# Performance work log

Hardware: AMD Instinct MI355X
Metric: run time of the kernel (lower is better)

Reference implementation:

```python
import jax, jax.numpy as jnp
import numpy as np

N_ACTIVE = 200000
GRID = 96
C_IN = 128
C_OUT = 128
K = 27  # 3x3x3 kernel offsets
BN_EPS = 1e-4  # scn.BatchNormalization default eps


def _build_rulebook(rng):
    """Sample N_ACTIVE unique voxels in a GRID^3 volume and build the
    submanifold-conv neighbor table: nbr_idx[k, i] = index of the active
    voxel at offset k from voxel i, or -1 if that site is inactive."""
    total = GRID ** 3
    flat = rng.choice(total, size=N_ACTIVE, replace=False).astype(np.int64)
    # flat -> dense lookup of active index
    lut = np.full(total, -1, dtype=np.int32)
    lut[flat] = np.arange(N_ACTIVE, dtype=np.int32)
    z = flat % GRID
    y = (flat // GRID) % GRID
    x = flat // (GRID * GRID)
    offs = np.array([(dx, dy, dz) for dx in (-1, 0, 1)
                     for dy in (-1, 0, 1) for dz in (-1, 0, 1)], dtype=np.int64)
    nbr = np.full((K, N_ACTIVE), -1, dtype=np.int32)
    for k, (dx, dy, dz) in enumerate(offs):
        nx, ny, nz = x + dx, y + dy, z + dz
        ok = ((nx >= 0) & (nx < GRID) & (ny >= 0) & (ny < GRID)
              & (nz >= 0) & (nz < GRID))
        nflat = np.where(ok, nx * GRID * GRID + ny * GRID + nz, 0)
        hit = np.where(ok, lut[nflat], -1)
        nbr[k] = hit
    return nbr


def setup_inputs() -> dict:
    key = jax.random.key(0)
    k1, k2 = jax.random.split(key)
    rng = np.random.default_rng(0)
    nbr_idx = jnp.asarray(_build_rulebook(rng))  # [27, N] int32
    features = jax.random.normal(k1, (N_ACTIVE, C_IN), dtype=jnp.float32)
    # Kaiming-ish scaled conv weights, one [Cin, Cout] matrix per offset
    W = jax.random.normal(k2, (K, C_IN, C_OUT), dtype=jnp.float32) * (
        1.0 / np.sqrt(K * C_IN))
    gamma = jnp.ones((C_OUT,), dtype=jnp.float32)
    beta = jnp.zeros((C_OUT,), dtype=jnp.float32)
    return {"features": features, "nbr_idx": nbr_idx, "W": W,
            "gamma": gamma, "beta": beta}


def reference(features, nbr_idx, W, gamma, beta):
    # --- Submanifold 3x3x3 convolution (gather -> GEMM -> accumulate) ---
    # Output sites == input sites; for each kernel offset k, gather the
    # neighbor's feature row (zero if inactive) and accumulate g @ W[k].
    out = jnp.zeros((features.shape[0], W.shape[-1]), dtype=features.dtype)
    for k in range(K):  # fixed small loop over 27 kernel offsets
        idx = nbr_idx[k]                         # [N]
        valid = (idx >= 0)
        g = features[jnp.maximum(idx, 0)]        # [N, Cin] irregular gather
        g = jnp.where(valid[:, None], g, 0.0)
        out = out + g @ W[k]                     # [N, Cout]
    # --- BatchNormalization over active sites (training batch stats) ---
    mean = jnp.mean(out, axis=0)
    var = jnp.mean(jnp.square(out - mean), axis=0)
    out = (out - mean) * (gamma * jax.lax.rsqrt(var + BN_EPS)) + beta
    # --- ReLU ---
    return jnp.maximum(out, 0.0)
```

## Files before the change

### kernel.cpp

```cpp
#include <hip/hip_runtime.h>
#include <hip/hip_bf16.h>
#include <cstdint>
#include <cstddef>

#define N_ACT 200000
#define CH 128
#define NOFF 27
#define TM 128

typedef __bf16 v8bf __attribute__((ext_vector_type(8)));
typedef float v4f __attribute__((ext_vector_type(4)));

__device__ __forceinline__ unsigned short f2bf(float f) {
    union { float f; unsigned int u; } x; x.f = f;
    unsigned int lsb = (x.u >> 16) & 1u;
    x.u += 0x7fffu + lsb;
    return (unsigned short)(x.u >> 16);
}

__global__ void cast_feat(const float* __restrict__ in,
                          unsigned short* __restrict__ out) {
    long long i = (long long)blockIdx.x * blockDim.x + threadIdx.x;
    long long base = i * 8;
    if (base >= (long long)N_ACT * CH) return;
    const float4* p = (const float4*)(in + base);
    float4 a = p[0], b = p[1];
    unsigned int w0 = (unsigned)f2bf(a.x) | ((unsigned)f2bf(a.y) << 16);
    unsigned int w1 = (unsigned)f2bf(a.z) | ((unsigned)f2bf(a.w) << 16);
    unsigned int w2 = (unsigned)f2bf(b.x) | ((unsigned)f2bf(b.y) << 16);
    unsigned int w3 = (unsigned)f2bf(b.z) | ((unsigned)f2bf(b.w) << 16);
    *(uint4*)(out + base) = make_uint4(w0, w1, w2, w3);
}

__global__ void prep_w(const float* __restrict__ W,
                       unsigned short* __restrict__ Wtp,
                       float* __restrict__ stats,
                       float* __restrict__ zpage) {
    int k = blockIdx.x;
    int t = threadIdx.x;
    if (k == 0 && t < 2 * CH) stats[t] = 0.0f;
    if (k == 0 && t < 64) zpage[t] = 0.0f;
    const float* wk = W + (size_t)k * CH * CH;
    for (int g = t; g < 2048; g += 256) {
        int q = g >> 9, r = g & 511;
        int jkk = r >> 6, lane = r & 63;
        int j = jkk >> 2, kk = jkk & 3;
        int lr = lane & 15, quad = lane >> 4;
        int cout = q * 32 + j * 16 + lr;
        int cin0 = kk * 32 + quad * 8;
        unsigned int wbuf[4];
        #pragma unroll
        for (int h = 0; h < 4; ++h) {
            unsigned short lo = f2bf(wk[(size_t)(cin0 + 2*h)     * CH + cout]);
            unsigned short hi = f2bf(wk[(size_t)(cin0 + 2*h + 1) * CH + cout]);
            wbuf[h] = (unsigned)lo | ((unsigned)hi << 16);
        }
        *(uint4*)(Wtp + ((size_t)(k * 4 + q) << 12) + (size_t)(jkk * 64 + lane) * 8)
            = make_uint4(wbuf[0], wbuf[1], wbuf[2], wbuf[3]);
    }
}

__global__ __launch_bounds__(256, 2) void conv_mfma(
        const unsigned short* __restrict__ feat,
        const int* __restrict__ nbr,
        const unsigned short* __restrict__ Wtp,
        const unsigned short* __restrict__ zpage,
        float* __restrict__ out,
        float* __restrict__ stats) {
    __shared__ __bf16 As[TM * CH];
    __shared__ int idxL[NOFF * TM];
    __shared__ float sred[256];

    const int t    = threadIdx.x;
    const int row0 = blockIdx.x * TM;
    const int wid  = t >> 6;
    const int lane = t & 63;
    const int lr   = lane & 15;
    const int quad = lane >> 4;

    for (int e = t; e < NOFF * TM; e += 256) {
        int k = e >> 7, r = e & 127;
        int gr = row0 + r;
        idxL[e] = (gr < N_ACT) ? nbr[(size_t)k * N_ACT + gr] : -1;
    }
    __syncthreads();

    v4f acc[8][2];
    #pragma unroll
    for (int i = 0; i < 8; ++i) {
        acc[i][0] = (v4f){0.f, 0.f, 0.f, 0.f};
        acc[i][1] = (v4f){0.f, 0.f, 0.f, 0.f};
    }

    const int sc  = t & 15;
    const int sr0 = t >> 4;
    const unsigned short* zsrc = zpage + sc * 8;

    v8bf B[8];

    auto stageA = [&](int k) {
        uint4 G[8];
        #pragma unroll
        for (int p = 0; p < 8; ++p) {
            int row = p * 16 + sr0;
            int idx = idxL[k * TM + row];
            const unsigned short* src =
                (idx >= 0) ? feat + ((size_t)idx << 7) + sc * 8 : zsrc;
            G[p] = *(const uint4*)src;
        }
        #pragma unroll
        for (int p = 0; p < 8; ++p) {
            int row = p * 16 + sr0;
            *(uint4*)(As + row * CH + (((sc + row) & 15) << 3)) = G[p];
        }
    };
    auto loadB = [&](int k) {
        const unsigned short* base =
            Wtp + ((size_t)(k * 4 + wid) << 12) + (size_t)lane * 8;
        #pragma unroll
        for (int jkk = 0; jkk < 8; ++jkk)
            B[jkk] = *(const v8bf*)(base + jkk * 512);
    };
    auto mfmaPhase = [&]() {
        #pragma unroll
        for (int i = 0; i < 8; ++i) {
            const __bf16* rowp = As + (i * 16 + lr) * CH;
            v8bf a[4];
            #pragma unroll
            for (int kk = 0; kk < 4; ++kk)
                a[kk] = *(const v8bf*)(rowp + (((kk * 4 + quad + lr) & 15) << 3));
            #pragma unroll
            for (int kk = 0; kk < 4; ++kk) {
                acc[i][0] = __builtin_amdgcn_mfma_f32_16x16x32_bf16(
                    a[kk], B[kk], acc[i][0], 0, 0, 0);
                acc[i][1] = __builtin_amdgcn_mfma_f32_16x16x32_bf16(
                    a[kk], B[4 + kk], acc[i][1], 0, 0, 0);
            }
        }
    };

    stageA(0);
    loadB(0);
    __syncthreads();

    #pragma unroll 1
    for (int k = 0; k < NOFF; ++k) {
        mfmaPhase();
        if (k + 1 < NOFF) {
            __syncthreads();
            stageA(k + 1);
            loadB(k + 1);
            __syncthreads();
        }
    }

    float psum[2] = {0.f, 0.f};
    float psq[2]  = {0.f, 0.f};
    #pragma unroll
    for (int i = 0; i < 8; ++i) {
        #pragma unroll
        for (int r = 0; r < 4; ++r) {
            int grow = row0 + i * 16 + quad * 4 + r;
            if (grow < N_ACT) {
                #pragma unroll
                for (int j = 0; j < 2; ++j) {
                    float v = acc[i][j][r];
                    out[(size_t)grow * CH + wid * 32 + j * 16 + lr] = v;
                    psum[j] += v;
                    psq[j]  += v * v;
                }
            }
        }
    }
    #pragma unroll
    for (int j = 0; j < 2; ++j) {
        psum[j] += __shfl_xor(psum[j], 16, 64);
        psq[j]  += __shfl_xor(psq[j], 16, 64);
        psum[j] += __shfl_xor(psum[j], 32, 64);
        psq[j]  += __shfl_xor(psq[j], 32, 64);
    }
    if (quad == 0) {
        #pragma unroll
        for (int j = 0; j < 2; ++j) {
            int c = wid * 32 + j * 16 + lr;
            sred[c]       = psum[j];
            sred[128 + c] = psq[j];
        }
    }
    __syncthreads();
    if (t < CH) {
        atomicAdd(&stats[t],      sred[t]);
        atomicAdd(&stats[CH + t], sred[128 + t]);
    }
}

__global__ void finalize_stats(const float* __restrict__ gamma,
                               const float* __restrict__ beta,
                               float* __restrict__ stats) {
    int c = threadIdx.x;
    if (c < CH) {
        float inv_n = 1.0f / (float)N_ACT;
        float mean  = stats[c] * inv_n;
        float var   = stats[CH + c] * inv_n - mean * mean;
        float sc    = gamma[c] * rsqrtf(var + 1e-4f);
        stats[2 * CH + c] = sc;
        stats[3 * CH + c] = beta[c] - mean * sc;
    }
}

__global__ void bn_relu(const float* __restrict__ conv,
                        const float* __restrict__ stats,
                        float* __restrict__ out) {
    long long i = (long long)blockIdx.x * blockDim.x + threadIdx.x;
    if (i >= (long long)N_ACT * CH / 4) return;
    int c4 = (int)(i & 31) * 4;
    float4 v  = ((const float4*)conv)[i];
    float4 sc = *(const float4*)(stats + 2 * CH + c4);
    float4 sh = *(const float4*)(stats + 3 * CH + c4);
    float4 o;
    o.x = fmaxf(v.x * sc.x + sh.x, 0.f);
    o.y = fmaxf(v.y * sc.y + sh.y, 0.f);
    o.z = fmaxf(v.z * sc.z + sh.z, 0.f);
    o.w = fmaxf(v.w * sc.w + sh.w, 0.f);
    ((float4*)out)[i] = o;
}

extern "C" void kernel_launch(void* const* d_in, const int* in_sizes, int n_in,
                              void* d_out, int out_size, void* d_ws, size_t ws_size,
                              hipStream_t stream) {
    const float* features = (const float*)d_in[0];
    const int*   nbr      = (const int*)d_in[1];
    const float* W        = (const float*)d_in[2];
    const float* gamma    = (const float*)d_in[3];
    const float* beta     = (const float*)d_in[4];
    float* outp = (float*)d_out;

    char* ws = (char*)d_ws;
    unsigned short* feat_bf = (unsigned short*)ws;
    unsigned short* Wtp     = (unsigned short*)(ws + 51200000);
    float* conv             = (float*)(ws + 51200000 + 884736);
    float* stats            = (float*)(ws + 51200000 + 884736 + 102400000);
    float* zpage            = stats + 4 * CH;

    cast_feat<<<12500, 256, 0, stream>>>(features, feat_bf);
    prep_w<<<NOFF, 256, 0, stream>>>(W, Wtp, stats, zpage);
    conv_mfma<<<(N_ACT + TM - 1) / TM, 256, 0, stream>>>(
        feat_bf, nbr, Wtp, (const unsigned short*)zpage, conv, stats);
    finalize_stats<<<1, CH, 0, stream>>>(gamma, beta, stats);
    bn_relu<<<25000, 256, 0, stream>>>(conv, stats, outp);
}
```

Baseline: 407.1 us.

## Retile conv MFMA warps to a 2x2 grid and use nontemporal output stores

Each of the four waves now computes a 64-row by 64-column tile instead of all 128 rows by 32 columns. That halves the per-wave LDS A-fragment reads while doubling the B fragments held in registers, and the per-block BN stat reduction is adjusted to sum over the two row halves. Separately, the conv output stores and the bn_relu load and store become nontemporal to reduce cache pollution on streaming data. The larger B register array (16 v8bf) plus 16 accumulators raises register pressure, which may threaten the 2-blocks-per-CU launch bound.

```diff
diff --git a/kernel.cpp b/kernel.cpp
--- a/kernel.cpp
+++ b/kernel.cpp
@@ -69,7 +69,7 @@
         float* __restrict__ stats) {
     __shared__ __bf16 As[TM * CH];
     __shared__ int idxL[NOFF * TM];
-    __shared__ float sred[256];
+    __shared__ float sred[512];
 
     const int t    = threadIdx.x;
     const int row0 = blockIdx.x * TM;
@@ -77,6 +77,8 @@
     const int lane = t & 63;
     const int lr   = lane & 15;
     const int quad = lane >> 4;
+    const int wr   = wid >> 1;
+    const int wc   = wid & 1;
 
     for (int e = t; e < NOFF * TM; e += 256) {
         int k = e >> 7, r = e & 127;
@@ -85,18 +87,18 @@
     }
     __syncthreads();
 
-    v4f acc[8][2];
+    v4f acc[4][4];
     #pragma unroll
-    for (int i = 0; i < 8; ++i) {
-        acc[i][0] = (v4f){0.f, 0.f, 0.f, 0.f};
-        acc[i][1] = (v4f){0.f, 0.f, 0.f, 0.f};
-    }
+    for (int i = 0; i < 4; ++i)
+        #pragma unroll
+        for (int j = 0; j < 4; ++j)
+            acc[i][j] = (v4f){0.f, 0.f, 0.f, 0.f};
 
     const int sc  = t & 15;
     const int sr0 = t >> 4;
     const unsigned short* zsrc = zpage + sc * 8;
 
-    v8bf B[8];
+    v8bf B[16];
 
     auto stageA = [&](int k) {
         uint4 G[8];
@@ -115,26 +117,30 @@
         }
     };
     auto loadB = [&](int k) {
-        const unsigned short* base =
-            Wtp + ((size_t)(k * 4 + wid) << 12) + (size_t)lane * 8;
-        #pragma unroll
-        for (int jkk = 0; jkk < 8; ++jkk)
-            B[jkk] = *(const v8bf*)(base + jkk * 512);
+        #pragma unroll
+        for (int j = 0; j < 4; ++j) {
+            const unsigned short* base = Wtp
+                + ((size_t)(k * 4 + 2 * wc + (j >> 1)) << 12)
+                + (size_t)(((j & 1) * 4) * 64 + lane) * 8;
+            #pragma unroll
+            for (int kk = 0; kk < 4; ++kk)
+                B[j * 4 + kk] = *(const v8bf*)(base + kk * 512);
+        }
     };
     auto mfmaPhase = [&]() {
         #pragma unroll
-        for (int i = 0; i < 8; ++i) {
-            const __bf16* rowp = As + (i * 16 + lr) * CH;
+        for (int i = 0; i < 4; ++i) {
+            const __bf16* rowp = As + (wr * 64 + i * 16 + lr) * CH;
             v8bf a[4];
             #pragma unroll
             for (int kk = 0; kk < 4; ++kk)
                 a[kk] = *(const v8bf*)(rowp + (((kk * 4 + quad + lr) & 15) << 3));
             #pragma unroll
             for (int kk = 0; kk < 4; ++kk) {
-                acc[i][0] = __builtin_amdgcn_mfma_f32_16x16x32_bf16(
-                    a[kk], B[kk], acc[i][0], 0, 0, 0);
-                acc[i][1] = __builtin_amdgcn_mfma_f32_16x16x32_bf16(
-                    a[kk], B[4 + kk], acc[i][1], 0, 0, 0);
+                #pragma unroll
+                for (int j = 0; j < 4; ++j)
+                    acc[i][j] = __builtin_amdgcn_mfma_f32_16x16x32_bf16(
+                        a[kk], B[j * 4 + kk], acc[i][j], 0, 0, 0);
             }
         }
     };
@@ -154,18 +160,19 @@
         }
     }
 
-    float psum[2] = {0.f, 0.f};
-    float psq[2]  = {0.f, 0.f};
+    float psum[4] = {0.f, 0.f, 0.f, 0.f};
+    float psq[4]  = {0.f, 0.f, 0.f, 0.f};
     #pragma unroll
-    for (int i = 0; i < 8; ++i) {
+    for (int i = 0; i < 4; ++i) {
         #pragma unroll
         for (int r = 0; r < 4; ++r) {
-            int grow = row0 + i * 16 + quad * 4 + r;
+            int grow = row0 + wr * 64 + i * 16 + quad * 4 + r;
             if (grow < N_ACT) {
                 #pragma unroll
-                for (int j = 0; j < 2; ++j) {
+                for (int j = 0; j < 4; ++j) {
                     float v = acc[i][j][r];
-                    out[(size_t)grow * CH + wid * 32 + j * 16 + lr] = v;
+                    __builtin_nontemporal_store(
+                        v, &out[(size_t)grow * CH + wc * 64 + j * 16 + lr]);
                     psum[j] += v;
                     psq[j]  += v * v;
                 }
@@ -173,7 +180,7 @@
         }
     }
     #pragma unroll
-    for (int j = 0; j < 2; ++j) {
+    for (int j = 0; j < 4; ++j) {
         psum[j] += __shfl_xor(psum[j], 16, 64);
         psq[j]  += __shfl_xor(psq[j], 16, 64);
         psum[j] += __shfl_xor(psum[j], 32, 64);
@@ -181,16 +188,16 @@
     }
     if (quad == 0) {
         #pragma unroll
-        for (int j = 0; j < 2; ++j) {
-            int c = wid * 32 + j * 16 + lr;
-            sred[c]       = psum[j];
-            sred[128 + c] = psq[j];
+        for (int j = 0; j < 4; ++j) {
+            int c = wc * 64 + j * 16 + lr;
+            sred[wr * CH + c]           = psum[j];
+            sred[2 * CH + wr * CH + c]  = psq[j];
         }
     }
     __syncthreads();
     if (t < CH) {
-        atomicAdd(&stats[t],      sred[t]);
-        atomicAdd(&stats[CH + t], sred[128 + t]);
+        atomicAdd(&stats[t],      sred[t] + sred[CH + t]);
+        atomicAdd(&stats[CH + t], sred[2 * CH + t] + sred[3 * CH + t]);
     }
 }
 
@@ -214,15 +221,15 @@
     long long i = (long long)blockIdx.x * blockDim.x + threadIdx.x;
     if (i >= (long long)N_ACT * CH / 4) return;
     int c4 = (int)(i & 31) * 4;
-    float4 v  = ((const float4*)conv)[i];
-    float4 sc = *(const float4*)(stats + 2 * CH + c4);
-    float4 sh = *(const float4*)(stats + 3 * CH + c4);
-    float4 o;
-    o.x = fmaxf(v.x * sc.x + sh.x, 0.f);
-    o.y = fmaxf(v.y * sc.y + sh.y, 0.f);
-    o.z = fmaxf(v.z * sc.z + sh.z, 0.f);
-    o.w = fmaxf(v.w * sc.w + sh.w, 0.f);
-    ((float4*)out)[i] = o;
+    v4f v  = __builtin_nontemporal_load((const v4f*)conv + i);
+    v4f sc = *(const v4f*)(stats + 2 * CH + c4);
+    v4f sh = *(const v4f*)(stats + 3 * CH + c4);
+    v4f o;
+    o[0] = fmaxf(v[0] * sc[0] + sh[0], 0.f);
+    o[1] = fmaxf(v[1] * sc[1] + sh[1], 0.f);
+    o[2] = fmaxf(v[2] * sc[2] + sh[2], 0.f);
+    o[3] = fmaxf(v[3] * sc[3] + sh[3], 0.f);
+    __builtin_nontemporal_store(o, (v4f*)out + i);
 }
 
 extern "C" void kernel_launch(void* const* d_in, const int* in_sizes, int n_in,
```

New measurement: 455.4 us. +11.9%, slower.
